# Performance work log

Hardware: AMD Instinct MI355X
Metric: run time of the kernel (lower is better)

## Reference

```python
import jax, jax.numpy as jnp
import numpy as np

BETA1, BETA2, BETA3 = 0.9, 0.8, 0.9
DECAY1, INC1 = 0.05, 5.0
DECAY3, INC3 = 0.05, 5.0
LATENCY = 4.0
B_CONST = 0.15
LIF1_MIN, LIF1_MAX = 150.0, 400.0
LIF3_MIN, LIF3_MAX = 50.0, 200.0
A_P, A_M, TAU_P, TAU_M = 0.01, 0.01, 20.0, 20.0  # exponential STDP params (params1/2/3)


def stdp(dt):
    # exponential STDP curve: potentiate when post fires after pre (dt>=0), depress otherwise
    return jnp.where(dt >= 0, A_P * jnp.exp(-dt / TAU_P), -A_M * jnp.exp(dt / TAU_M))


def setup_inputs() -> dict:
    key = jax.random.key(0)
    k1, k2, k3, k4 = jax.random.split(key, 4)
    H, N, C = 8192, 4096, 128
    return {
        "image": jax.random.uniform(k1, (N,), jnp.float32),
        "W1": jax.random.uniform(k2, (H, N), jnp.float32),
        "W2": jax.random.uniform(k3, (N, H), jnp.float32),
        "W3": jax.random.uniform(k4, (C, N), jnp.float32),
        "thr1": 100.0 * jnp.ones((H,), jnp.float32),
        "thr2": 5.0 * jnp.ones((N,), jnp.float32),
        "thr3": 100.0 * jnp.ones((C,), jnp.float32),
        "time": 256,
        "pw": 8,
    }


def reference(image, W1, W2, W3, thr1, thr2, thr3, time, pw):
    N = image.shape[0]
    H = W1.shape[0]
    C = W3.shape[0]
    T = int(time)
    Tf = jnp.float32(T)

    img_t = Tf * image  # input spike times, [N]
    # rate -> pulse encoding: input_spikes[t, i] = 1 for t in [floor(img_t[i]), floor(img_t[i])+pw)
    t_axis = jnp.arange(T, dtype=jnp.float32)[:, None]          # [T,1]
    start = jnp.floor(img_t)[None, :]                            # [1,N]
    input_spikes = ((t_axis >= start) & (t_axis < start + pw)).astype(jnp.float32)  # [T,N]

    def wta(mem, th):
        # winner-take-all (snntorch inhibition=True): only argmax neuron may spike
        j = jnp.argmax(mem)
        fire = (mem[j] > th[j]).astype(mem.dtype)
        return fire * jax.nn.one_hot(j, mem.shape[0], dtype=mem.dtype)

    def step(carry, xs):
        mem1, mem2, mem3, th1, th3, r1, r2, r3, hid_act, out_act = carry
        x, t = xs
        # layer 1: Leaky LIF, inhibition, reset-to-zero
        mem1 = BETA1 * mem1 + jnp.dot(W1, x)
        spk1 = wta(mem1, th1)
        mem1 = mem1 * (1.0 - spk1)
        # layer 2: Leaky LIF, no inhibition, reset-by-subtract
        mem2 = BETA2 * mem2 + jnp.dot(W2, spk1)
        spk2 = (mem2 > thr2).astype(mem2.dtype)
        mem2 = mem2 - spk2 * thr2
        # layer 3 (clustering): Leaky LIF, inhibition, zeroed after any spike
        mem3 = BETA3 * mem3 + jnp.dot(W3, spk2)
        spk3 = wta(mem3, th3)
        mem3 = mem3 - spk3 * th3
        mem3 = jnp.where(jnp.sum(spk3) > 0, 0.0, mem3)
        # first-spike-time recon (recon stays at first nonzero spk*(t+1))
        r1 = jnp.where(r1 != 0, r1, spk1 * (t + 1.0))
        r2 = jnp.where(r2 != 0, r2, spk2 * (t + 1.0))
        r3 = jnp.where(r3 != 0, r3, spk3 * (t + 1.0))
        hid_act = hid_act + spk1
        out_act = out_act + spk2
        # adaptive thresholds: homeostatic decay + spike-triggered increase, clamped
        th1 = jnp.clip(th1 - DECAY1 + INC1 * spk1, LIF1_MIN, LIF1_MAX)
        th3 = jnp.clip(th3 - DECAY3 + INC3 * spk3, LIF3_MIN, LIF3_MAX)
        return (mem1, mem2, mem3, th1, th3, r1, r2, r3, hid_act, out_act), None

    z = jnp.zeros
    carry0 = (z(H), z(N), z(C), thr1, thr3, z(H), z(N), z(C), z(H), z(N))
    (mem1, mem2, mem3, th1, th3, r1, r2, r3, hid_act, out_act), _ = jax.lax.scan(
        step, carry0, (input_spikes, jnp.arange(T, dtype=jnp.float32)))

    # neurons that never spiked get time T
    r1 = jnp.where(r1 == 0, Tf, r1)
    r2 = jnp.where(r2 == 0, Tf, r2)
    r3 = jnp.where(r3 == 0, Tf, r3)

    # STDP weight updates (exponential), same structure as PresentImage
    hid_mask = (hid_act > 0).astype(jnp.float32)
    delta_t1 = (r1[:, None] - img_t[None, :]) * hid_mask[:, None]      # [H,N]
    W1_new = W1 + stdp(delta_t1)
    delta_t2 = r2[:, None] - r1[None, :]                                # [N,H]
    zeta = (Tf - r1) * hid_mask / Tf                                    # [H]
    rho = (r2 - LATENCY - img_t) / Tf + B_CONST                         # [N]
    W2_new = jnp.clip(W2 + stdp(delta_t2) * (rho[:, None] * zeta[None, :]), 0.0, 1.0)
    delta_t3 = r3[:, None] - r2[None, :]                                # [C,N]
    W3_new = W3 + stdp(delta_t3)

    error = (img_t - (r2 - LATENCY)) / Tf
    error_scalar = jnp.sum(jnp.square(error))
    return (error, error_scalar, r1, r2, r3, W1_new, W2_new, W3_new)
```

## Files before the change

### kernel.cpp

```cpp
#include <hip/hip_runtime.h>
#include <cstdint>
#include <cstddef>

#define Hn 8192
#define Nn 4096
#define Cn 128
#define Tt 256
#define CAP 192

typedef unsigned long long ull;

__device__ __forceinline__ float th_lazy2(float b, float lo, float hi, int nup){
    if (nup <= 0) return b;
    float a = fminf(fmaxf(__fsub_rn(b, 0.05f), lo), hi);
    if (nup == 1) return a;
    return fmaxf(__fsub_rn(a, __fmul_rn(0.05f, (float)(nup - 1))), lo);
}

__device__ __forceinline__ float clamp01(float v){
    return fminf(fmaxf(v, 0.f), 1.f);
}

template<int CTRL>
__device__ __forceinline__ int dpp_i(int x, int old){
    return __builtin_amdgcn_update_dpp(old, x, CTRL, 0xf, 0xf, false);
}
__device__ __forceinline__ float wave_max_f(float v){
    const int NEG = __float_as_int(-3.4e38f);
#define STEPM(C) { float o = __int_as_float(dpp_i<C>(__float_as_int(v), NEG)); v = fmaxf(v, o); }
    STEPM(0x111) STEPM(0x112) STEPM(0x114) STEPM(0x118) STEPM(0x142) STEPM(0x143)
#undef STEPM
    return __int_as_float(__builtin_amdgcn_readlane(__float_as_int(v), 63));
}
__device__ __forceinline__ int wave_argmax_l(float bv, int bh, float &wv, int &wh){
    float v = wave_max_f(bv);
    ull tie = __ballot(bv == v);
    int tl = __ffsll((long long)tie) - 1;
    int h = __builtin_amdgcn_readlane(bh, tl);
    if (__builtin_expect(__popcll(tie) > 1, 0)){
        ull m = tie & (tie - 1);
        while (m){
            int l2 = __ffsll((long long)m) - 1;
            int h2 = __builtin_amdgcn_readlane(bh, l2);
            if (h2 < h){ h = h2; tl = l2; }
            m &= m - 1;
        }
    }
    wv = v; wh = h; return tl;
}
__device__ __forceinline__ float rl_f(float x, int l){
    return __int_as_float(__builtin_amdgcn_readlane(__float_as_int(x), l));
}

__global__ __launch_bounds__(1024) void k_prep(const float* __restrict__ image,
        int* __restrict__ boff, int* __restrict__ sidx, unsigned* __restrict__ anyv){
    __shared__ int s_start[Nn];
    __shared__ int s_c4[4][Tt];
    __shared__ int s_boff[Tt + 1];
    int tid = threadIdx.x;
    for (int i = tid; i < Nn; i += 1024)
        s_start[i] = (int)floorf(__fmul_rn(256.f, image[i]));
    if (tid < Tt) anyv[tid] = 0u;
    __syncthreads();
    int b = tid & 255, q = tid >> 8;
    {
        int c = 0;
        for (int k = 0; k < 1024; ++k) c += (s_start[q * 1024 + k] == b) ? 1 : 0;
        s_c4[q][b] = c;
    }
    __syncthreads();
    if (tid == 0){
        int acc = 0;
        for (int bb = 0; bb < Tt; ++bb){
            s_boff[bb] = acc;
            acc += s_c4[0][bb] + s_c4[1][bb] + s_c4[2][bb] + s_c4[3][bb];
        }
        s_boff[Tt] = acc;
    }
    __syncthreads();
    if (tid <= Tt) boff[tid] = s_boff[tid];
    int p = s_boff[b];
    if (q > 0) p += s_c4[0][b];
    if (q > 1) p += s_c4[1][b];
    if (q > 2) p += s_c4[2][b];
    for (int k = 0; k < 1024; ++k){
        int i = q * 1024 + k;
        if (s_start[i] == b) sidx[p++] = i;
    }
}

__global__ __launch_bounds__(256) void k_gbuckets(const float* __restrict__ W1,
        const int* __restrict__ boff, const int* __restrict__ sidx,
        float* __restrict__ G_T){
    __shared__ float rows[2][Nn];
    int tid = threadIdx.x;
    int h0 = blockIdx.x * 2;
    for (int r = 0; r < 2; ++r){
        const float4* src = (const float4*)(W1 + (size_t)(h0 + r) * Nn);
        float4* dst = (float4*)rows[r];
        for (int j = tid; j < Nn / 4; j += 256) dst[j] = src[j];
    }
    __syncthreads();
    int t = tid;
    int b0 = boff[t], b1 = boff[t + 1];
    float s0 = 0.f, s1 = 0.f;
    for (int k = b0; k < b1; ++k){
        int i = sidx[k];
        s0 += rows[0][i]; s1 += rows[1][i];
    }
    G_T[(size_t)(h0 + 0) * Tt + t] = s0;
    G_T[(size_t)(h0 + 1) * Tt + t] = s1;
}

__global__ __launch_bounds__(256) void k_c1M(const float* __restrict__ G_T,
        float* __restrict__ M, float* __restrict__ r1pre, float* __restrict__ o_r1){
    __shared__ float tile[32][Tt + 1];
    __shared__ float c1s[32][Tt + 1];
    const int tid = threadIdx.x;
    const int h0 = blockIdx.x * 32;
    for (int r = 0; r < 32; ++r) tile[r][tid] = G_T[(size_t)(h0 + r) * Tt + tid];
    __syncthreads();
    {
        int hs = tid & 31, ts = tid >> 5;
        for (int tb = 0; tb < 32; ++tb){
            int t = tb * 8 + ts;
            int lo = (t - 7 < 0) ? 0 : t - 7;
            float s = 0.f;
            for (int u = lo; u <= t; ++u) s += tile[hs][u];
            c1s[hs][t] = s;
        }
    }
    __syncthreads();
    if (tid < 32){
        float m = 0.f;
        for (int t = 0; t < Tt; ++t){
            m = __fadd_rn(__fmul_rn(0.9f, m), c1s[tid][t]);
            M[(size_t)t * Hn + h0 + tid] = m;
        }
        r1pre[h0 + tid] = 0.f;
        o_r1[h0 + tid] = 256.f;
    }
}

__global__ __launch_bounds__(256) void k_sel(const float* __restrict__ M,
        float4* __restrict__ cand){
    const int t = blockIdx.x, tid = threadIdx.x;
    __shared__ float s_row[Hn];
    __shared__ unsigned s_hist[256];
    __shared__ unsigned s_suf[256];
    __shared__ unsigned s_pref;
    __shared__ int s_rank;
    __shared__ int s_cnt;
    __shared__ int s_idx[CAP + 64];
    {
        const float4* src = (const float4*)(M + (size_t)t * Hn);
        float4* d4 = (float4*)s_row;
        for (int j = tid; j < Hn / 4; j += 256) d4[j] = src[j];
    }
    if (tid == 0){ s_pref = 0u; s_rank = CAP; s_cnt = 0; }
    __syncthreads();
#pragma unroll
    for (int b = 3; b >= 0; --b){
        s_hist[tid] = 0u;
        __syncthreads();
        unsigned pref = s_pref;
        int r = s_rank;
        for (int k = 0; k < 32; ++k){
            unsigned u = __float_as_uint(s_row[tid + (k << 8)]);
            bool match = (b == 3) ? true : ((u >> ((b + 1) * 8)) == pref);
            if (match) atomicAdd(&s_hist[(u >> (b * 8)) & 255], 1u);
        }
        __syncthreads();
        s_suf[tid] = s_hist[tid];
        __syncthreads();
#pragma unroll
        for (int off = 1; off < 256; off <<= 1){
            unsigned v = (tid + off < 256) ? s_suf[tid + off] : 0u;
            __syncthreads();
            s_suf[tid] += v;
            __syncthreads();
        }
        unsigned above = s_suf[tid] - s_hist[tid];
        if ((int)above < r && r <= (int)s_suf[tid]){
            s_pref = (pref << 8) | (unsigned)tid;
            s_rank = r - (int)above;
        }
        __syncthreads();
    }
    unsigned V = s_pref;
    for (int k = 0; k < 32; ++k){
        int i = tid + (k << 8);
        unsigned u = __float_as_uint(s_row[i]);
        if (u >= V){
            int p = atomicAdd(&s_cnt, 1);
            if (p < CAP + 64) s_idx[p] = i;
        }
    }
    __syncthreads();
    int c = s_cnt;
    bool ovf = (c > CAP);
    float vV = ovf ? 3.4e38f : __uint_as_float(V);
    for (int i = tid; i < CAP; i += 256){
        float4 e;
        if (!ovf && i < c){
            int ix = s_idx[i];
            e = make_float4(s_row[ix], __int_as_float(ix | (1 << 15)), 0.f, vV);
        } else {
            e = make_float4(-1.f, 0.f, 0.f, vV);
        }
        cand[(size_t)t * CAP + i] = e;
    }
}

#define NB_W1 1024
#define NB_W2 1024
#define NB_W3T 128

union FusedLDS {
    struct {
        float4 mst[Hn];
        int j1[Tt];
        unsigned bm[256];
    } w;
    float tl[64][65];
};

__global__ __launch_bounds__(512, 1) void k_fused(
        const float* __restrict__ M, const float4* __restrict__ cand,
        const float* __restrict__ thr1,
        const float* __restrict__ W1, const float* __restrict__ W2,
        const float* __restrict__ W3,
        float* __restrict__ o_W1, float* __restrict__ o_W2, float* __restrict__ W3T,
        float* __restrict__ r1pre, float* __restrict__ o_r1,
        int* __restrict__ j1s, int* __restrict__ mh, int* __restrict__ nRout){
    __shared__ FusedLDS u;
    const int bid = blockIdx.x;
    const int tid = threadIdx.x;

    if (bid >= 1 && bid < 1 + NB_W1){
        size_t base = (size_t)(bid - 1) * 8192;
        const float4* src = (const float4*)W1;
        float4* dst = (float4*)o_W1;
        for (int i = tid; i < 8192; i += 2048){
            float4 a0 = src[base + i];
            float4 a1 = src[base + i + 512];
            float4 a2 = src[base + i + 1024];
            float4 a3 = src[base + i + 1536];
            a0.x = __fadd_rn(a0.x, 0.01f); a0.y = __fadd_rn(a0.y, 0.01f);
            a0.z = __fadd_rn(a0.z, 0.01f); a0.w = __fadd_rn(a0.w, 0.01f);
            a1.x = __fadd_rn(a1.x, 0.01f); a1.y = __fadd_rn(a1.y, 0.01f);
            a1.z = __fadd_rn(a1.z, 0.01f); a1.w = __fadd_rn(a1.w, 0.01f);
            a2.x = __fadd_rn(a2.x, 0.01f); a2.y = __fadd_rn(a2.y, 0.01f);
            a2.z = __fadd_rn(a2.z, 0.01f); a2.w = __fadd_rn(a2.w, 0.01f);
            a3.x = __fadd_rn(a3.x, 0.01f); a3.y = __fadd_rn(a3.y, 0.01f);
            a3.z = __fadd_rn(a3.z, 0.01f); a3.w = __fadd_rn(a3.w, 0.01f);
            dst[base + i]        = a0;
            dst[base + i + 512]  = a1;
            dst[base + i + 1024] = a2;
            dst[base + i + 1536] = a3;
        }
        return;
    }
    if (bid >= 1 + NB_W1 && bid < 1 + NB_W1 + NB_W2){
        size_t base = (size_t)(bid - 1 - NB_W1) * 8192;
        const float4* src = (const float4*)W2;
        float4* dst = (float4*)o_W2;
        for (int i = tid; i < 8192; i += 2048){
            float4 a0 = src[base + i];
            float4 a1 = src[base + i + 512];
            float4 a2 = src[base + i + 1024];
            float4 a3 = src[base + i + 1536];
            a0.x = clamp01(a0.x); a0.y = clamp01(a0.y); a0.z = clamp01(a0.z); a0.w = clamp01(a0.w);
            a1.x = clamp01(a1.x); a1.y = clamp01(a1.y); a1.z = clamp01(a1.z); a1.w = clamp01(a1.w);
            a2.x = clamp01(a2.x); a2.y = clamp01(a2.y); a2.z = clamp01(a2.z); a2.w = clamp01(a2.w);
            a3.x = clamp01(a3.x); a3.y = clamp01(a3.y); a3.z = clamp01(a3.z); a3.w = clamp01(a3.w);
            dst[base + i]        = a0;
            dst[base + i + 512]  = a1;
            dst[base + i + 1024] = a2;
            dst[base + i + 1536] = a3;
        }
        return;
    }
    if (bid >= 1 + NB_W1 + NB_W2){
        int r = bid - 1 - NB_W1 - NB_W2;
        int bx = r & 63, by = r >> 6;
        int n0 = bx * 64, c0 = by * 64;
        for (int e = tid; e < 64 * 64; e += 512){
            int rr = e >> 6, cc = e & 63;
            u.tl[rr][cc] = W3[(size_t)(c0 + rr) * Nn + n0 + cc];
        }
        __syncthreads();
        for (int e = tid; e < 64 * 64; e += 512){
            int rn = e >> 6, cc = e & 63;
            W3T[(size_t)(n0 + rn) * Cn + c0 + cc] = u.tl[cc][rn];
        }
        return;
    }

    for (int h = tid; h < Hn; h += 512)
        u.w.mst[h] = make_float4(0.f, -1.f, thr1[h], 0.f);
    __syncthreads();
    if (tid >= 64) return;
    const int lane = tid;
    const float Lc = -0.15200309344504997f;

    float4 cA0 = cand[lane],         cA1 = cand[64 + lane],         cA2 = cand[128 + lane];
    float4 cB0 = cand[CAP + lane],   cB1 = cand[CAP + 64 + lane],   cB2 = cand[CAP + 128 + lane];
    float4 cC0 = cand[2*CAP + lane], cC1 = cand[2*CAP + 64 + lane], cC2 = cand[2*CAP + 128 + lane];
    float4 gA0, gA1, gA2;
    {
        int h0 = __float_as_int(cA0.y) & 8191;
        int h1 = __float_as_int(cA1.y) & 8191;
        int h2 = __float_as_int(cA2.y) & 8191;
        gA0 = u.w.mst[h0]; gA1 = u.w.mst[h1]; gA2 = u.w.mst[h2];
    }

    for (int t = 0; t < Tt; ++t){
        const float tf = (float)t;
        float bm = -3.4e38f; int bhh = 0x7FFFFFFF;
        float braw = 0.f, bts = 0.f, bthb = 0.f;
#define CPROC(c) { \
        int mc = __float_as_int(cA##c.y); \
        int hc = mc & 8191; \
        float dd = __fsub_rn(tf, gA##c.y); \
        float mem = __fsub_rn(cA##c.x, __fmul_rn(exp2f(__fmul_rn(dd, Lc)), gA##c.x)); \
        if (!((mc >> 15) & 1)) mem = -3.4e38f; \
        if (mem > bm || (mem == bm && hc < bhh)){ bm = mem; bhh = hc; braw = cA##c.x; bts = gA##c.y; bthb = gA##c.z; } }
        CPROC(0) CPROC(1) CPROC(2)
#undef CPROC
        const int hB0 = __float_as_int(cB0.y) & 8191;
        const int hB1 = __float_as_int(cB1.y) & 8191;
        const int hB2 = __float_as_int(cB2.y) & 8191;
        float4 gB0 = u.w.mst[hB0];
        float4 gB1 = u.w.mst[hB1];
        float4 gB2 = u.w.mst[hB2];
        float wv; int wh;
        int wl = wave_argmax_l(bm, bhh, wv, wh);
        float raw = rl_f(braw, wl), tsv = rl_f(bts, wl), thb = rl_f(bthb, wl);
        const float vc = cA0.w;
        int skip = 0;
        if (__builtin_expect(wv < vc, 0)){
            if (t > 0 && vc < 150.f){
                skip = 1;
            } else {
                float fv = -3.4e38f; int fh = 0x7FFFFFFF;
                float fraw = 0.f, fts = 0.f, fthb = 0.f;
                const float4* Mrow4 = (const float4*)(M + (size_t)t * Hn);
                for (int q = 0; q < 32; ++q){
                    int e = q * 64 + lane;
                    float4 mv = Mrow4[e];
                    int ib = e * 4;
                    float4 g0 = u.w.mst[ib+0], g1 = u.w.mst[ib+1], g2 = u.w.mst[ib+2], g3 = u.w.mst[ib+3];
#define FPROC(comp, gg, o2) { float x = mv.comp; float dd = __fsub_rn(tf, gg.y); \
                    float mm = __fsub_rn(x, __fmul_rn(exp2f(__fmul_rn(dd, Lc)), gg.x)); \
                    int h2 = ib + o2; \
                    if (mm > fv || (mm == fv && h2 < fh)){ fv = mm; fh = h2; fraw = x; fts = gg.y; fthb = gg.z; } }
                    FPROC(x, g0, 0) FPROC(y, g1, 1) FPROC(z, g2, 2) FPROC(w, g3, 3)
#undef FPROC
                }
                wl = wave_argmax_l(fv, fh, wv, wh);
                raw = rl_f(fraw, wl); tsv = rl_f(fts, wl); thb = rl_f(fthb, wl);
            }
        }
        int fire = 0; float thnew = 0.f;
        if (!skip){
            float te = th_lazy2(thb, 150.f, 400.f, t - (int)tsv - 1);
            if (wv > te){
                fire = 1;
                thnew = fminf(fmaxf(__fadd_rn(__fsub_rn(te, 0.05f), 5.0f), 150.f), 400.f);
            }
        }
        if (fire){
            if (lane == 0){
                u.w.j1[t] = wh;
                if (tsv < 0.f){ o_r1[wh] = tf + 1.f; r1pre[wh] = tf + 1.f; }
                u.w.mst[wh] = make_float4(raw, tf, thnew, 0.f);
            }
            float4 upd = make_float4(raw, tf, thnew, 0.f);
            if (hB0 == wh) gB0 = upd;
            if (hB1 == wh) gB1 = upd;
            if (hB2 == wh) gB2 = upd;
        } else {
            if (lane == 0) u.w.j1[t] = -1;
        }
        cA0 = cB0; cA1 = cB1; cA2 = cB2;
        cB0 = cC0; cB1 = cC1; cB2 = cC2;
        int tn = (t + 3 < Tt) ? t + 3 : Tt - 1;
        cC0 = cand[(size_t)tn * CAP + lane];
        cC1 = cand[(size_t)tn * CAP + 64 + lane];
        cC2 = cand[(size_t)tn * CAP + 128 + lane];
        gA0 = gB0; gA1 = gB1; gA2 = gB2;
    }

    for (int i = lane; i < 256; i += 64) u.w.bm[i] = 0u;
    asm volatile("s_waitcnt lgkmcnt(0)" ::: "memory");
    for (int i = lane; i < Tt; i += 64){
        int h = u.w.j1[i];
        j1s[i] = h;
        if (h >= 0) atomicOr(&u.w.bm[h >> 5], 1u << (h & 31));
    }
    asm volatile("s_waitcnt lgkmcnt(0)" ::: "memory");
    unsigned w0 = u.w.bm[lane*4+0], w1 = u.w.bm[lane*4+1];
    unsigned w2 = u.w.bm[lane*4+2], w3 = u.w.bm[lane*4+3];
    int c = __popc(w0) + __popc(w1) + __popc(w2) + __popc(w3);
    int inc = c;
#pragma unroll
    for (int off = 1; off < 64; off <<= 1){
        int v = __shfl_up(inc, off);
        if (lane >= off) inc += v;
    }
    int b = inc - c;
#define WALK(wrd, k) { unsigned ww = wrd; while (ww){ int bt = __ffs(ww) - 1; ww &= ww - 1; \
        mh[b++] = ((lane * 4 + k) << 5) | bt; } }
    WALK(w0, 0) WALK(w1, 1) WALK(w2, 2) WALK(w3, 3)
#undef WALK
    if (lane == 63) *nRout = inc;
}

__global__ __launch_bounds__(64) void k_lif2(const float* __restrict__ W2,
        const int* __restrict__ j1s, const float* __restrict__ thr2,
        float* __restrict__ o_r2, ull* __restrict__ spkb, unsigned* __restrict__ anyv){
    __shared__ int s_j[Tt];
    int lane = threadIdx.x, blk = blockIdx.x;
    for (int i = lane; i < Tt; i += 64) s_j[i] = j1s[i];
    __syncthreads();
    int n = blk * 64 + lane;
    const float* Wrow = W2 + (size_t)n * Hn;
    float tv = thr2[n], m = 0.f, rp = 0.f;
#define LD(dst, tt) { int hh = s_j[tt]; dst = (hh >= 0) ? Wrow[hh] : 0.f; }
#define STEP(uu, tt) { m = __fadd_rn(__fmul_rn(0.8f, m), uu); int f = 0; \
        if (m > tv){ m = __fsub_rn(m, tv); if (rp == 0.f) rp = (float)((tt) + 1); f = 1; } \
        ull mask = __ballot(f); \
        if (lane == 0){ spkb[(tt) * 64 + blk] = mask; if (mask) atomicOr(&anyv[tt], 1u); } }
    float u0, u1, u2, u3;
    LD(u0, 0) LD(u1, 1) LD(u2, 2) LD(u3, 3)
    for (int g = 0; g < 64; ++g){
        float v0 = 0.f, v1 = 0.f, v2 = 0.f, v3 = 0.f;
        if (g < 63){
            int bb = (g + 1) * 4;
            LD(v0, bb) LD(v1, bb + 1) LD(v2, bb + 2) LD(v3, bb + 3)
        }
        int t = g * 4;
        STEP(u0, t) STEP(u1, t + 1) STEP(u2, t + 2) STEP(u3, t + 3)
        u0 = v0; u1 = v1; u2 = v2; u3 = v3;
    }
#undef LD
#undef STEP
    o_r2[n] = (rp == 0.f) ? 256.f : rp;
}

__global__ __launch_bounds__(128, 1) void k_sim3(const ull* __restrict__ spkb,
        const unsigned* __restrict__ anyv, const float* __restrict__ W3T,
        const float* __restrict__ thr3, float* __restrict__ o_r3){
    int tid = threadIdx.x, lane = tid & 63, w = tid >> 6;
    __shared__ unsigned s_any[Tt];
    __shared__ ull s_r2[2];
    __shared__ int s_fire;
    for (int i = tid; i < Tt; i += 128) s_any[i] = anyv[i];
    float m = 0.f, th0 = thr3[tid], rp = 0.f, thv = 0.f;
    int ts = -1, zero = 1;
    __syncthreads();
    for (int t = 0; t < Tt; ++t){
        if (zero && s_any[t] == 0u) continue;
        float d = 0.f;
        if (s_any[t]){
            for (int ww = 0; ww < 64; ++ww){
                ull bits = spkb[t * 64 + ww];
                while (bits){
                    int b2 = __ffsll((long long)bits) - 1;
                    bits &= bits - 1;
                    d = __fadd_rn(d, W3T[(size_t)(ww * 64 + b2) * Cn + tid]);
                }
            }
        }
        m = __fadd_rn(__fmul_rn(0.9f, m), d);
        ull k = (((ull)__float_as_uint(m >= 0.f ? m : 0.f)) << 32) | (unsigned)(8191 - tid);
        if (!(m >= 0.f)) k = (unsigned)(8191 - tid);
#pragma unroll
        for (int off = 32; off >= 1; off >>= 1){
            ull o = __shfl_down(k, off);
            if (o > k) k = o;
        }
        if (lane == 0) s_r2[w] = k;
        __syncthreads();
        ull wk = s_r2[0] > s_r2[1] ? s_r2[0] : s_r2[1];
        int wc = 8191 - (int)(wk & 0xFFFFu);
        float wv = __uint_as_float((unsigned)(wk >> 32));
        if (tid == wc){
            float te = (ts < 0) ? th_lazy2(th0, 50.f, 200.f, t)
                                : th_lazy2(thv, 50.f, 200.f, t - ts - 1);
            int f = (wv > te) ? 1 : 0;
            s_fire = f;
            if (f){
                thv = fminf(fmaxf(__fadd_rn(__fsub_rn(te, 0.05f), 5.0f), 50.f), 200.f);
                ts = t;
                if (rp == 0.f) rp = (float)(t + 1);
            }
        }
        __syncthreads();
        if (s_fire){ m = 0.f; zero = 1; }
        else zero = 0;
        __syncthreads();
    }
    o_r3[tid] = (rp == 0.f) ? 256.f : rp;
}

__global__ __launch_bounds__(1024) void k_scalars(const float* __restrict__ image,
        const float* __restrict__ r1pre, const float* __restrict__ o_r1,
        const float* __restrict__ o_r2,
        float* __restrict__ zeta, float* __restrict__ rho,
        float* __restrict__ imgt, float* __restrict__ eiP, float* __restrict__ eiM,
        float* __restrict__ Pv, float* __restrict__ Qv,
        float* __restrict__ E2P, float* __restrict__ E2M,
        float* __restrict__ o_err, float* __restrict__ o_es){
    int tid = threadIdx.x;
    for (int h = tid; h < Hn; h += 1024){
        float r1f = o_r1[h];
        float mask = (r1pre[h] != 0.f) ? 1.f : 0.f;
        float z = __fmul_rn(__fmul_rn(__fsub_rn(256.f, r1f), mask), 0.00390625f);
        zeta[h] = z;
        Pv[h] = __expf(r1f * 0.05f) * z;
        Qv[h] = __expf(-r1f * 0.05f) * z;
    }
    float acc = 0.f;
    for (int n = tid; n < Nn; n += 1024){
        float img = __fmul_rn(256.f, image[n]);
        float r2f = o_r2[n];
        float e = __fmul_rn(__fsub_rn(img, __fsub_rn(r2f, 4.0f)), 0.00390625f);
        o_err[n] = e;
        rho[n] = __fadd_rn(__fmul_rn(__fsub_rn(__fsub_rn(r2f, 4.0f), img), 0.00390625f), 0.15f);
        imgt[n] = img;
        eiP[n] = __expf(img * 0.05f);
        eiM[n] = __expf(-img * 0.05f);
        E2P[n] = __expf(r2f * 0.05f);
        E2M[n] = __expf(-r2f * 0.05f);
        acc = __fadd_rn(acc, __fmul_rn(e, e));
    }
    __shared__ float red[16];
    for (int off = 32; off >= 1; off >>= 1) acc += __shfl_down(acc, off);
    int lane = tid & 63, w = tid >> 6;
    if (lane == 0) red[w] = acc;
    __syncthreads();
    if (tid == 0){
        float s = 0.f;
        for (int q = 0; q < 16; ++q) s += red[q];
        *o_es = s;
    }
}

__global__ __launch_bounds__(256) void k_w1fix(const float* __restrict__ W1,
        const float* __restrict__ imgt, const float* __restrict__ eiP,
        const float* __restrict__ eiM, const float* __restrict__ o_r1,
        const int* __restrict__ mh, const int* __restrict__ nRout,
        float* __restrict__ o_W1){
    int slot = blockIdx.x;
    if (slot >= *nRout) return;
    int h = mh[slot];
    int tid = threadIdx.x;
    float r1f = o_r1[h];
    float a = 0.01f * __expf(-r1f * 0.05f);
    float b = 0.01f * __expf( r1f * 0.05f);
    const float4* src = (const float4*)(W1 + (size_t)h * Nn);
    float4* dst = (float4*)(o_W1 + (size_t)h * Nn);
    const float4* ig = (const float4*)imgt;
    const float4* p4 = (const float4*)eiP;
    const float4* m4 = (const float4*)eiM;
    for (int i = tid; i < Nn / 4; i += 256){
        float4 s = src[i];
        float4 im = ig[i], pp = p4[i], mm = m4[i];
        s.x += (r1f >= im.x) ? a * pp.x : -(b * mm.x);
        s.y += (r1f >= im.y) ? a * pp.y : -(b * mm.y);
        s.z += (r1f >= im.z) ? a * pp.z : -(b * mm.z);
        s.w += (r1f >= im.w) ? a * pp.w : -(b * mm.w);
        dst[i] = s;
    }
}

__global__ __launch_bounds__(128) void k_w2fix(
        const float* __restrict__ o_r1, const float* __restrict__ Pv,
        const float* __restrict__ Qv, const float* __restrict__ o_r2,
        const float* __restrict__ rho, const int* __restrict__ mh,
        const int* __restrict__ nRout, float* __restrict__ o_W2){
    __shared__ int   s_h[Tt];
    __shared__ float s_rv[Tt], s_pp[Tt], s_qq[Tt];
    int n = blockIdx.x, tid = threadIdx.x;
    int nRv = *nRout;
    for (int s = tid; s < nRv; s += 128){
        int h = mh[s];
        s_h[s] = h; s_rv[s] = o_r1[h]; s_pp[s] = Pv[h]; s_qq[s] = Qv[h];
    }
    __syncthreads();
    float r2f = o_r2[n], rh = rho[n];
    float A = 0.01f * rh * __expf(-r2f * 0.05f);
    float B = 0.01f * rh * __expf( r2f * 0.05f);
    for (int s = tid; s < nRv; s += 128){
        size_t idx = (size_t)n * Hn + s_h[s];
        float w = o_W2[idx];
        float rv = s_rv[s];
        w = clamp01(w + ((r2f >= rv) ? A * s_pp[s] : -(B * s_qq[s])));
        o_W2[idx] = w;
    }
}

__global__ __launch_bounds__(256) void k_w3new(const float* __restrict__ W3,
        const float* __restrict__ o_r2, const float* __restrict__ E2P,
        const float* __restrict__ E2M, const float* __restrict__ o_r3,
        float* __restrict__ o_W3){
    int c = blockIdx.x, tid = threadIdx.x;
    float r3f = o_r3[c];
    float a = 0.01f * __expf(-r3f * 0.05f);
    float b = 0.01f * __expf( r3f * 0.05f);
    const float4* src = (const float4*)(W3 + (size_t)c * Nn);
    float4* dst = (float4*)(o_W3 + (size_t)c * Nn);
    const float4* r24 = (const float4*)o_r2;
    const float4* p4 = (const float4*)E2P;
    const float4* m4 = (const float4*)E2M;
    for (int i = tid; i < Nn / 4; i += 256){
        float4 s = src[i]; float4 rv = r24[i]; float4 pp = p4[i]; float4 mm = m4[i];
        s.x += (r3f >= rv.x) ? a * pp.x : -(b * mm.x);
        s.y += (r3f >= rv.y) ? a * pp.y : -(b * mm.y);
        s.z += (r3f >= rv.z) ? a * pp.z : -(b * mm.z);
        s.w += (r3f >= rv.w) ? a * pp.w : -(b * mm.w);
        dst[i] = s;
    }
}

extern "C" void kernel_launch(void* const* d_in, const int* in_sizes, int n_in,
                              void* d_out, int out_size, void* d_ws, size_t ws_size,
                              hipStream_t stream){
    const float* image = (const float*)d_in[0];
    const float* W1   = (const float*)d_in[1];
    const float* W2   = (const float*)d_in[2];
    const float* W3   = (const float*)d_in[3];
    const float* thr1 = (const float*)d_in[4];
    const float* thr2 = (const float*)d_in[5];
    const float* thr3 = (const float*)d_in[6];

    float* out  = (float*)d_out;
    float* o_err = out;
    float* o_es  = out + 4096;
    float* o_r1  = out + 4097;
    float* o_r2  = out + 12289;
    float* o_r3  = out + 16385;
    float* o_W1  = out + 16513;
    float* o_W2  = o_W1 + (size_t)Hn * Nn;
    float* o_W3  = o_W2 + (size_t)Nn * Hn;

    float* ws = (float*)d_ws;
    float* G_T   = ws;
    float* M     = G_T + (size_t)Hn * Tt;
    float* W3T   = M + (size_t)Tt * Hn;
    float4* cand = (float4*)(W3T + (size_t)Nn * Cn);
    ull* spkb    = (ull*)(cand + (size_t)Tt * CAP);
    float* r1pre = (float*)(spkb + (size_t)Tt * 64);
    float* zeta  = r1pre + Hn;
    float* rho   = zeta + Hn;
    float* imgt  = rho + Nn;
    float* eiP   = imgt + Nn;
    float* eiM   = eiP + Nn;
    float* Pv    = eiM + Nn;
    float* Qv    = Pv + Hn;
    float* E2P   = Qv + Hn;
    float* E2M   = E2P + Nn;
    int* boff   = (int*)(E2M + Nn);
    int* sidx   = boff + (Tt + 1);
    int* j1s    = sidx + Nn;
    int* mh     = j1s + Tt;
    int* nRout  = mh + 256;
    unsigned* anyv = (unsigned*)(nRout + 1);

    k_prep<<<1, 1024, 0, stream>>>(image, boff, sidx, anyv);
    k_gbuckets<<<Hn / 2, 256, 0, stream>>>(W1, boff, sidx, G_T);
    k_c1M<<<Hn / 32, 256, 0, stream>>>(G_T, M, r1pre, o_r1);
    k_sel<<<Tt, 256, 0, stream>>>(M, cand);
    k_fused<<<1 + NB_W1 + NB_W2 + NB_W3T, 512, 0, stream>>>(
        M, cand, thr1, W1, W2, W3, o_W1, o_W2, W3T, r1pre, o_r1, j1s, mh, nRout);
    k_lif2<<<Nn / 64, 64, 0, stream>>>(W2, j1s, thr2, o_r2, spkb, anyv);
    k_sim3<<<1, 128, 0, stream>>>(spkb, anyv, W3T, thr3, o_r3);
    k_scalars<<<1, 1024, 0, stream>>>(image, r1pre, o_r1, o_r2, zeta, rho,
                                      imgt, eiP, eiM, Pv, Qv, E2P, E2M, o_err, o_es);
    k_w1fix<<<256, 256, 0, stream>>>(W1, imgt, eiP, eiM, o_r1, mh, nRout, o_W1);
    k_w2fix<<<Nn, 128, 0, stream>>>(o_r1, Pv, Qv, o_r2, rho, mh, nRout, o_W2);
    k_w3new<<<Cn, 256, 0, stream>>>(W3, o_r2, E2P, E2M, o_r3, o_W3);
}
```

Measured before the change: 506.8 us.

## Split W1 bulk copy out of fused kernel and merge post-processing kernels

Moves the W1+0.01 bulk copy into its own kernel launched right after the bucket pass, leaving k_fused to handle only the W2 clamp and W3 transpose with smaller per-block chunks. The scalar, W1-fix and W3-update kernels are merged into one multi-role kernel, with the image exponentials moved into k_prep and the r2 exponentials computed inline, which removes launches and the E2P/E2M buffers. k_sim3 now stages the spike bitmaps in shared memory. The risks are extra exp work in the W3 path and the loss of any overlap between the W1 copy and the serial work in k_fused.

```diff
diff --git a/kernel.cpp b/kernel.cpp
--- a/kernel.cpp
+++ b/kernel.cpp
@@ -53,13 +53,20 @@
 }
 
 __global__ __launch_bounds__(1024) void k_prep(const float* __restrict__ image,
-        int* __restrict__ boff, int* __restrict__ sidx, unsigned* __restrict__ anyv){
+        int* __restrict__ boff, int* __restrict__ sidx, unsigned* __restrict__ anyv,
+        float* __restrict__ imgt, float* __restrict__ eiP, float* __restrict__ eiM){
     __shared__ int s_start[Nn];
     __shared__ int s_c4[4][Tt];
     __shared__ int s_boff[Tt + 1];
     int tid = threadIdx.x;
-    for (int i = tid; i < Nn; i += 1024)
-        s_start[i] = (int)floorf(__fmul_rn(256.f, image[i]));
+    for (int i = tid; i < Nn; i += 1024){
+        float im = image[i];
+        float img = __fmul_rn(256.f, im);
+        s_start[i] = (int)floorf(img);
+        imgt[i] = img;
+        eiP[i] = __expf(img * 0.05f);
+        eiM[i] = __expf(-img * 0.05f);
+    }
     if (tid < Tt) anyv[tid] = 0u;
     __syncthreads();
     int b = tid & 255, q = tid >> 8;
@@ -110,6 +117,19 @@
     }
     G_T[(size_t)(h0 + 0) * Tt + t] = s0;
     G_T[(size_t)(h0 + 1) * Tt + t] = s1;
+}
+
+__global__ __launch_bounds__(256) void k_w1bulk(const float* __restrict__ W1,
+        float* __restrict__ o_W1){
+    size_t base = (size_t)blockIdx.x * 4096;
+    const float4* src = (const float4*)W1;
+    float4* dst = (float4*)o_W1;
+    for (int i = threadIdx.x; i < 4096; i += 256){
+        float4 s = src[base + i];
+        s.x = __fadd_rn(s.x, 0.01f); s.y = __fadd_rn(s.y, 0.01f);
+        s.z = __fadd_rn(s.z, 0.01f); s.w = __fadd_rn(s.w, 0.01f);
+        dst[base + i] = s;
+    }
 }
 
 __global__ __launch_bounds__(256) void k_c1M(const float* __restrict__ G_T,
@@ -212,8 +232,7 @@
     }
 }
 
-#define NB_W1 1024
-#define NB_W2 1024
+#define NB_W2 2048
 #define NB_W3T 128
 
 union FusedLDS {
@@ -228,44 +247,19 @@
 __global__ __launch_bounds__(512, 1) void k_fused(
         const float* __restrict__ M, const float4* __restrict__ cand,
         const float* __restrict__ thr1,
-        const float* __restrict__ W1, const float* __restrict__ W2,
-        const float* __restrict__ W3,
-        float* __restrict__ o_W1, float* __restrict__ o_W2, float* __restrict__ W3T,
+        const float* __restrict__ W2, const float* __restrict__ W3,
+        float* __restrict__ o_W2, float* __restrict__ W3T,
         float* __restrict__ r1pre, float* __restrict__ o_r1,
         int* __restrict__ j1s, int* __restrict__ mh, int* __restrict__ nRout){
     __shared__ FusedLDS u;
     const int bid = blockIdx.x;
     const int tid = threadIdx.x;
 
-    if (bid >= 1 && bid < 1 + NB_W1){
-        size_t base = (size_t)(bid - 1) * 8192;
-        const float4* src = (const float4*)W1;
-        float4* dst = (float4*)o_W1;
-        for (int i = tid; i < 8192; i += 2048){
-            float4 a0 = src[base + i];
-            float4 a1 = src[base + i + 512];
-            float4 a2 = src[base + i + 1024];
-            float4 a3 = src[base + i + 1536];
-            a0.x = __fadd_rn(a0.x, 0.01f); a0.y = __fadd_rn(a0.y, 0.01f);
-            a0.z = __fadd_rn(a0.z, 0.01f); a0.w = __fadd_rn(a0.w, 0.01f);
-            a1.x = __fadd_rn(a1.x, 0.01f); a1.y = __fadd_rn(a1.y, 0.01f);
-            a1.z = __fadd_rn(a1.z, 0.01f); a1.w = __fadd_rn(a1.w, 0.01f);
-            a2.x = __fadd_rn(a2.x, 0.01f); a2.y = __fadd_rn(a2.y, 0.01f);
-            a2.z = __fadd_rn(a2.z, 0.01f); a2.w = __fadd_rn(a2.w, 0.01f);
-            a3.x = __fadd_rn(a3.x, 0.01f); a3.y = __fadd_rn(a3.y, 0.01f);
-            a3.z = __fadd_rn(a3.z, 0.01f); a3.w = __fadd_rn(a3.w, 0.01f);
-            dst[base + i]        = a0;
-            dst[base + i + 512]  = a1;
-            dst[base + i + 1024] = a2;
-            dst[base + i + 1536] = a3;
-        }
-        return;
-    }
-    if (bid >= 1 + NB_W1 && bid < 1 + NB_W1 + NB_W2){
-        size_t base = (size_t)(bid - 1 - NB_W1) * 8192;
+    if (bid >= 1 && bid < 1 + NB_W2){
+        size_t base = (size_t)(bid - 1) * 4096;
         const float4* src = (const float4*)W2;
         float4* dst = (float4*)o_W2;
-        for (int i = tid; i < 8192; i += 2048){
+        for (int i = tid; i < 4096; i += 2048){
             float4 a0 = src[base + i];
             float4 a1 = src[base + i + 512];
             float4 a2 = src[base + i + 1024];
@@ -281,8 +275,8 @@
         }
         return;
     }
-    if (bid >= 1 + NB_W1 + NB_W2){
-        int r = bid - 1 - NB_W1 - NB_W2;
+    if (bid >= 1 + NB_W2){
+        int r = bid - 1 - NB_W2;
         int bx = r & 63, by = r >> 6;
         int n0 = bx * 64, c0 = by * 64;
         for (int e = tid; e < 64 * 64; e += 512){
@@ -453,9 +447,15 @@
         const unsigned* __restrict__ anyv, const float* __restrict__ W3T,
         const float* __restrict__ thr3, float* __restrict__ o_r3){
     int tid = threadIdx.x, lane = tid & 63, w = tid >> 6;
+    __shared__ ull s_spk[Tt * 64];
     __shared__ unsigned s_any[Tt];
     __shared__ ull s_r2[2];
     __shared__ int s_fire;
+    {
+        const uint4* src = (const uint4*)spkb;
+        uint4* dst = (uint4*)s_spk;
+        for (int i = tid; i < Tt * 64 / 2; i += 128) dst[i] = src[i];
+    }
     for (int i = tid; i < Tt; i += 128) s_any[i] = anyv[i];
     float m = 0.f, th0 = thr3[tid], rp = 0.f, thv = 0.f;
     int ts = -1, zero = 1;
@@ -465,7 +465,7 @@
         float d = 0.f;
         if (s_any[t]){
             for (int ww = 0; ww < 64; ++ww){
-                ull bits = spkb[t * 64 + ww];
+                ull bits = s_spk[t * 64 + ww];
                 while (bits){
                     int b2 = __ffsll((long long)bits) - 1;
                     bits &= bits - 1;
@@ -505,74 +505,84 @@
     o_r3[tid] = (rp == 0.f) ? 256.f : rp;
 }
 
-__global__ __launch_bounds__(1024) void k_scalars(const float* __restrict__ image,
+__global__ __launch_bounds__(256) void k_post(const float* __restrict__ image,
         const float* __restrict__ r1pre, const float* __restrict__ o_r1,
-        const float* __restrict__ o_r2,
+        const float* __restrict__ o_r2, const float* __restrict__ o_r3,
+        const float* __restrict__ imgt, const float* __restrict__ eiP,
+        const float* __restrict__ eiM,
+        const float* __restrict__ W1, const float* __restrict__ W3,
+        const int* __restrict__ mh, const int* __restrict__ nRout,
         float* __restrict__ zeta, float* __restrict__ rho,
-        float* __restrict__ imgt, float* __restrict__ eiP, float* __restrict__ eiM,
         float* __restrict__ Pv, float* __restrict__ Qv,
-        float* __restrict__ E2P, float* __restrict__ E2M,
-        float* __restrict__ o_err, float* __restrict__ o_es){
-    int tid = threadIdx.x;
-    for (int h = tid; h < Hn; h += 1024){
+        float* __restrict__ o_err, float* __restrict__ o_es,
+        float* __restrict__ o_W1, float* __restrict__ o_W3){
+    const int bid = blockIdx.x;
+    const int tid = threadIdx.x;
+    if (bid == 0){
+        for (int h = tid; h < Hn; h += 256){
+            float r1f = o_r1[h];
+            float mask = (r1pre[h] != 0.f) ? 1.f : 0.f;
+            float z = __fmul_rn(__fmul_rn(__fsub_rn(256.f, r1f), mask), 0.00390625f);
+            zeta[h] = z;
+            Pv[h] = __expf(r1f * 0.05f) * z;
+            Qv[h] = __expf(-r1f * 0.05f) * z;
+        }
+        float acc = 0.f;
+        for (int n = tid; n < Nn; n += 256){
+            float img = __fmul_rn(256.f, image[n]);
+            float r2f = o_r2[n];
+            float e = __fmul_rn(__fsub_rn(img, __fsub_rn(r2f, 4.0f)), 0.00390625f);
+            o_err[n] = e;
+            rho[n] = __fadd_rn(__fmul_rn(__fsub_rn(__fsub_rn(r2f, 4.0f), img), 0.00390625f), 0.15f);
+            acc = __fadd_rn(acc, __fmul_rn(e, e));
+        }
+        __shared__ float red[4];
+        for (int off = 32; off >= 1; off >>= 1) acc += __shfl_down(acc, off);
+        int lane = tid & 63, w = tid >> 6;
+        if (lane == 0) red[w] = acc;
+        __syncthreads();
+        if (tid == 0) *o_es = red[0] + red[1] + red[2] + red[3];
+        return;
+    }
+    if (bid <= 256){
+        int slot = bid - 1;
+        if (slot >= *nRout) return;
+        int h = mh[slot];
         float r1f = o_r1[h];
-        float mask = (r1pre[h] != 0.f) ? 1.f : 0.f;
-        float z = __fmul_rn(__fmul_rn(__fsub_rn(256.f, r1f), mask), 0.00390625f);
-        zeta[h] = z;
-        Pv[h] = __expf(r1f * 0.05f) * z;
-        Qv[h] = __expf(-r1f * 0.05f) * z;
-    }
-    float acc = 0.f;
-    for (int n = tid; n < Nn; n += 1024){
-        float img = __fmul_rn(256.f, image[n]);
-        float r2f = o_r2[n];
-        float e = __fmul_rn(__fsub_rn(img, __fsub_rn(r2f, 4.0f)), 0.00390625f);
-        o_err[n] = e;
-        rho[n] = __fadd_rn(__fmul_rn(__fsub_rn(__fsub_rn(r2f, 4.0f), img), 0.00390625f), 0.15f);
-        imgt[n] = img;
-        eiP[n] = __expf(img * 0.05f);
-        eiM[n] = __expf(-img * 0.05f);
-        E2P[n] = __expf(r2f * 0.05f);
-        E2M[n] = __expf(-r2f * 0.05f);
-        acc = __fadd_rn(acc, __fmul_rn(e, e));
-    }
-    __shared__ float red[16];
-    for (int off = 32; off >= 1; off >>= 1) acc += __shfl_down(acc, off);
-    int lane = tid & 63, w = tid >> 6;
-    if (lane == 0) red[w] = acc;
-    __syncthreads();
-    if (tid == 0){
-        float s = 0.f;
-        for (int q = 0; q < 16; ++q) s += red[q];
-        *o_es = s;
-    }
-}
-
-__global__ __launch_bounds__(256) void k_w1fix(const float* __restrict__ W1,
-        const float* __restrict__ imgt, const float* __restrict__ eiP,
-        const float* __restrict__ eiM, const float* __restrict__ o_r1,
-        const int* __restrict__ mh, const int* __restrict__ nRout,
-        float* __restrict__ o_W1){
-    int slot = blockIdx.x;
-    if (slot >= *nRout) return;
-    int h = mh[slot];
-    int tid = threadIdx.x;
-    float r1f = o_r1[h];
-    float a = 0.01f * __expf(-r1f * 0.05f);
-    float b = 0.01f * __expf( r1f * 0.05f);
-    const float4* src = (const float4*)(W1 + (size_t)h * Nn);
-    float4* dst = (float4*)(o_W1 + (size_t)h * Nn);
-    const float4* ig = (const float4*)imgt;
-    const float4* p4 = (const float4*)eiP;
-    const float4* m4 = (const float4*)eiM;
-    for (int i = tid; i < Nn / 4; i += 256){
-        float4 s = src[i];
-        float4 im = ig[i], pp = p4[i], mm = m4[i];
-        s.x += (r1f >= im.x) ? a * pp.x : -(b * mm.x);
-        s.y += (r1f >= im.y) ? a * pp.y : -(b * mm.y);
-        s.z += (r1f >= im.z) ? a * pp.z : -(b * mm.z);
-        s.w += (r1f >= im.w) ? a * pp.w : -(b * mm.w);
-        dst[i] = s;
+        float a = 0.01f * __expf(-r1f * 0.05f);
+        float b = 0.01f * __expf( r1f * 0.05f);
+        const float4* src = (const float4*)(W1 + (size_t)h * Nn);
+        float4* dst = (float4*)(o_W1 + (size_t)h * Nn);
+        const float4* ig = (const float4*)imgt;
+        const float4* p4 = (const float4*)eiP;
+        const float4* m4 = (const float4*)eiM;
+        for (int i = tid; i < Nn / 4; i += 256){
+            float4 s = src[i];
+            float4 im = ig[i], pp = p4[i], mm = m4[i];
+            s.x += (r1f >= im.x) ? a * pp.x : -(b * mm.x);
+            s.y += (r1f >= im.y) ? a * pp.y : -(b * mm.y);
+            s.z += (r1f >= im.z) ? a * pp.z : -(b * mm.z);
+            s.w += (r1f >= im.w) ? a * pp.w : -(b * mm.w);
+            dst[i] = s;
+        }
+        return;
+    }
+    {
+        int cc = bid - 257;
+        float r3f = o_r3[cc];
+        float a = 0.01f * __expf(-r3f * 0.05f);
+        float b = 0.01f * __expf( r3f * 0.05f);
+        const float4* src = (const float4*)(W3 + (size_t)cc * Nn);
+        float4* dst = (float4*)(o_W3 + (size_t)cc * Nn);
+        const float4* r24 = (const float4*)o_r2;
+        for (int i = tid; i < Nn / 4; i += 256){
+            float4 s = src[i]; float4 rv = r24[i];
+            s.x += (r3f >= rv.x) ? a * __expf(rv.x * 0.05f) : -(b * __expf(-rv.x * 0.05f));
+            s.y += (r3f >= rv.y) ? a * __expf(rv.y * 0.05f) : -(b * __expf(-rv.y * 0.05f));
+            s.z += (r3f >= rv.z) ? a * __expf(rv.z * 0.05f) : -(b * __expf(-rv.z * 0.05f));
+            s.w += (r3f >= rv.w) ? a * __expf(rv.w * 0.05f) : -(b * __expf(-rv.w * 0.05f));
+            dst[i] = s;
+        }
     }
 }
 
@@ -599,29 +609,6 @@
         float rv = s_rv[s];
         w = clamp01(w + ((r2f >= rv) ? A * s_pp[s] : -(B * s_qq[s])));
         o_W2[idx] = w;
-    }
-}
-
-__global__ __launch_bounds__(256) void k_w3new(const float* __restrict__ W3,
-        const float* __restrict__ o_r2, const float* __restrict__ E2P,
-        const float* __restrict__ E2M, const float* __restrict__ o_r3,
-        float* __restrict__ o_W3){
-    int c = blockIdx.x, tid = threadIdx.x;
-    float r3f = o_r3[c];
-    float a = 0.01f * __expf(-r3f * 0.05f);
-    float b = 0.01f * __expf( r3f * 0.05f);
-    const float4* src = (const float4*)(W3 + (size_t)c * Nn);
-    float4* dst = (float4*)(o_W3 + (size_t)c * Nn);
-    const float4* r24 = (const float4*)o_r2;
-    const float4* p4 = (const float4*)E2P;
-    const float4* m4 = (const float4*)E2M;
-    for (int i = tid; i < Nn / 4; i += 256){
-        float4 s = src[i]; float4 rv = r24[i]; float4 pp = p4[i]; float4 mm = m4[i];
-        s.x += (r3f >= rv.x) ? a * pp.x : -(b * mm.x);
-        s.y += (r3f >= rv.y) ? a * pp.y : -(b * mm.y);
-        s.z += (r3f >= rv.z) ? a * pp.z : -(b * mm.z);
-        s.w += (r3f >= rv.w) ? a * pp.w : -(b * mm.w);
-        dst[i] = s;
     }
 }
 
@@ -660,26 +647,23 @@
     float* eiM   = eiP + Nn;
     float* Pv    = eiM + Nn;
     float* Qv    = Pv + Hn;
-    float* E2P   = Qv + Hn;
-    float* E2M   = E2P + Nn;
-    int* boff   = (int*)(E2M + Nn);
+    int* boff   = (int*)(Qv + Hn);
     int* sidx   = boff + (Tt + 1);
     int* j1s    = sidx + Nn;
     int* mh     = j1s + Tt;
     int* nRout  = mh + 256;
     unsigned* anyv = (unsigned*)(nRout + 1);
 
-    k_prep<<<1, 1024, 0, stream>>>(image, boff, sidx, anyv);
+    k_prep<<<1, 1024, 0, stream>>>(image, boff, sidx, anyv, imgt, eiP, eiM);
     k_gbuckets<<<Hn / 2, 256, 0, stream>>>(W1, boff, sidx, G_T);
+    k_w1bulk<<<2048, 256, 0, stream>>>(W1, o_W1);
     k_c1M<<<Hn / 32, 256, 0, stream>>>(G_T, M, r1pre, o_r1);
     k_sel<<<Tt, 256, 0, stream>>>(M, cand);
-    k_fused<<<1 + NB_W1 + NB_W2 + NB_W3T, 512, 0, stream>>>(
-        M, cand, thr1, W1, W2, W3, o_W1, o_W2, W3T, r1pre, o_r1, j1s, mh, nRout);
+    k_fused<<<1 + NB_W2 + NB_W3T, 512, 0, stream>>>(
+        M, cand, thr1, W2, W3, o_W2, W3T, r1pre, o_r1, j1s, mh, nRout);
     k_lif2<<<Nn / 64, 64, 0, stream>>>(W2, j1s, thr2, o_r2, spkb, anyv);
     k_sim3<<<1, 128, 0, stream>>>(spkb, anyv, W3T, thr3, o_r3);
-    k_scalars<<<1, 1024, 0, stream>>>(image, r1pre, o_r1, o_r2, zeta, rho,
-                                      imgt, eiP, eiM, Pv, Qv, E2P, E2M, o_err, o_es);
-    k_w1fix<<<256, 256, 0, stream>>>(W1, imgt, eiP, eiM, o_r1, mh, nRout, o_W1);
+    k_post<<<1 + 256 + 128, 256, 0, stream>>>(image, r1pre, o_r1, o_r2, o_r3,
+        imgt, eiP, eiM, W1, W3, mh, nRout, zeta, rho, Pv, Qv, o_err, o_es, o_W1, o_W3);
     k_w2fix<<<Nn, 128, 0, stream>>>(o_r1, Pv, Qv, o_r2, rho, mh, nRout, o_W2);
-    k_w3new<<<Cn, 256, 0, stream>>>(W3, o_r2, E2P, E2M, o_r3, o_W3);
-}
+}
```

Result: slower. 560.7 us (+10.6%).
